# Kernel tuning notes

Hardware: AMD Instinct MI355X
Metric: run time of the kernel (lower is better)

Reference implementation:

```python
import jax, jax.numpy as jnp
import numpy as np

B, N, NH, H = 32, 512, 4, 32      # batch, agents per group, heads, hidden per head
IN_DIM, OUT_DIM = 128, 128
BIG = 9.0e15
SQRT_DK = float(np.sqrt(H))


def setup_inputs() -> dict:
    key = jax.random.key(0)
    keys = iter(jax.random.split(key, 64))

    def nrm(shape, scale=0.05):
        return jax.random.normal(next(keys), shape, dtype=jnp.float32) * scale

    inp = {}
    inp["x0"] = jax.random.normal(next(keys), (B, N, IN_DIM), dtype=jnp.float32)
    inp["x1"] = jax.random.normal(next(keys), (B, N, IN_DIM), dtype=jnp.float32)
    for name in ("m00", "m01", "m10", "m11"):
        inp[name] = jax.random.randint(next(keys), (B, N, N), 0, 2, dtype=jnp.int32)
    # per-group q/k/v projections: Linear(in_dim, NH*H)
    for g in (0, 1):
        inp[f"wq{g}"] = nrm((IN_DIM, NH * H)); inp[f"bq{g}"] = nrm((NH * H,))
        inp[f"wk{g}"] = nrm((IN_DIM, NH * H)); inp[f"bk{g}"] = nrm((NH * H,))
        inp[f"wv{g}"] = nrm((IN_DIM, NH * H)); inp[f"bv{g}"] = nrm((NH * H,))
    # fc_outs[i][j]: Linear(NH*H, H)
    for i in (0, 1):
        for j in (0, 1):
            inp[f"wo{i}{j}"] = nrm((NH * H, H)); inp[f"bo{i}{j}"] = nrm((H,))
    # fc_out_final[i]: Linear(H * 2, out_dim)
    for g in (0, 1):
        inp[f"wf{g}"] = nrm((2 * H, OUT_DIM)); inp[f"bf{g}"] = nrm((OUT_DIM,))
    return inp


def _qkv(x, wq, bq, wk, bk, wv, bv):
    q = jax.nn.relu(x @ wq + bq)
    k = jax.nn.relu(x @ wk + bk)
    v = jax.nn.relu(x @ wv + bv)
    return q, k, v


def _split_heads(t):
    # [B, N, NH*H] -> [B, NH, N, H]; contiguous H-blocks == torch per-head slices
    return t.reshape(B, t.shape[1], NH, H).transpose(0, 2, 1, 3)


def _attend(q, k, v, mask, gate):
    qh, kh, vh = _split_heads(q), _split_heads(k), _split_heads(v)
    logits = jnp.einsum('bhqd,bhkd->bhqk', qh, kh) / SQRT_DK
    m = mask.astype(logits.dtype)[:, None]            # [B,1,Nq,Nk]
    w = jax.nn.softmax(logits * m - BIG * (1.0 - m), axis=-1)
    if gate:
        has = (mask.sum(axis=-1) > 0).astype(w.dtype)  # [B,Nq]
        w = w * has[:, None, :, None]
    out = jnp.einsum('bhqk,bhkd->bhqd', w, vh)
    # heads concatenated along feature dim (matches torch.cat of head slices)
    return out.transpose(0, 2, 1, 3).reshape(B, q.shape[1], NH * H)


def reference(x0, x1, m00, m01, m10, m11,
              wq0, bq0, wk0, bk0, wv0, bv0,
              wq1, bq1, wk1, bk1, wv1, bv1,
              wo00, bo00, wo01, bo01, wo10, bo10, wo11, bo11,
              wf0, bf0, wf1, bf1):
    q0, k0, v0 = _qkv(x0, wq0, bq0, wk0, bk0, wv0, bv0)
    q1, k1, v1 = _qkv(x1, wq1, bq1, wk1, bk1, wv1, bv1)
    inner0 = jax.nn.relu(_attend(q0, k0, v0, m00, gate=False) @ wo00 + bo00)
    inner1 = jax.nn.relu(_attend(q1, k1, v1, m11, gate=False) @ wo11 + bo11)
    inter0 = jax.nn.relu(_attend(q0, k1, v1, m01, gate=True) @ wo01 + bo01)
    inter1 = jax.nn.relu(_attend(q1, k0, v0, m10, gate=True) @ wo10 + bo10)
    out0 = jnp.concatenate([inner0, inter0], axis=-1) @ wf0 + bf0
    out1 = jnp.concatenate([inner1, inter1], axis=-1) @ wf1 + bf1
    return (out0, out1)
```

## Files before the change

kernel.cpp:

```cpp
#include <hip/hip_runtime.h>

#define B_    32
#define N_    512
#define D_    128
#define ROWS  (B_ * N_)
#define SCALE_ 0.17677669529663687f

typedef __bf16 bf16x8 __attribute__((ext_vector_type(8)));
typedef __bf16 bf16x4 __attribute__((ext_vector_type(4)));
typedef float  f32x4  __attribute__((ext_vector_type(4)));

static __device__ __forceinline__ f32x4 mfma16(bf16x8 a, bf16x8 b, f32x4 c) {
  return __builtin_amdgcn_mfma_f32_16x16x32_bf16(a, b, c, 0, 0, 0);
}

__global__ __launch_bounds__(256) void prep_kernel(
    const int* __restrict__ m00, const int* __restrict__ m01,
    const int* __restrict__ m10, const int* __restrict__ m11,
    const float* __restrict__ wq0, const float* __restrict__ wk0, const float* __restrict__ wv0,
    const float* __restrict__ wq1, const float* __restrict__ wk1, const float* __restrict__ wv1,
    const float* __restrict__ wo00, const float* __restrict__ wo01,
    const float* __restrict__ wo10, const float* __restrict__ wo11,
    const float* __restrict__ wf0, const float* __restrict__ wf1,
    __bf16* __restrict__ wtb, __bf16* __restrict__ wob, __bf16* __restrict__ wfb,
    unsigned long long* __restrict__ mpk)
{
  const int bx = blockIdx.x, t = threadIdx.x;
  if (bx < 2048) {
    const int wid = bx * 4 + (t >> 6);
    const int lane = t & 63;
    const int rg = wid & 7, ch = (wid >> 3) & 7, b = (wid >> 6) & 31, a = wid >> 11;
    const int* msel = (a == 0) ? m00 : (a == 1) ? m11 : (a == 2) ? m01 : m10;
    const int* src = msel + ((size_t)b * N_ + rg * 64) * N_ + ch * 64 + lane;
    unsigned long long mine = 0;
    #pragma unroll 8
    for (int it = 0; it < 64; ++it) {
      int v = src[(size_t)it * N_];
      unsigned long long bits = __ballot(v != 0);
      if (it == lane) mine = bits;
    }
    mpk[((size_t)(a * 32 + b) * 8 + ch) * 512 + rg * 64 + lane] = mine;
  } else if (bx < 2054) {
    const int mat = bx - 2048;
    const float* w = (mat == 0) ? wq0 : (mat == 1) ? wk0 : (mat == 2) ? wv0
                   : (mat == 3) ? wq1 : (mat == 4) ? wk1 : wv1;
    __bf16* dst = wtb + mat * 16384;
    for (int idx = t; idx < 16384; idx += 256) {
      const int k = idx >> 7, n = idx & 127;
      dst[n * 128 + k] = (__bf16)w[idx];
    }
  } else if (bx < 2058) {
    const int i = bx - 2054;
    const float* w = (i == 0) ? wo00 : (i == 1) ? wo11 : (i == 2) ? wo01 : wo10;
    __bf16* dst = wob + i * 4096;
    for (int idx = t; idx < 4096; idx += 256) {
      const int k = idx >> 5, n = idx & 31;
      dst[n * 128 + k] = (__bf16)w[idx];
    }
  } else {
    const int g = bx - 2058;
    const float* w = g ? wf1 : wf0;
    __bf16* dst = wfb + g * 8192;
    for (int idx = t; idx < 8192; idx += 256) {
      const int n = idx >> 6, k = idx & 63;
      dst[n * 64 + k] = (__bf16)w[(size_t)k * 128 + n];
    }
  }
}

__global__ __launch_bounds__(256) void qkv_kernel(
    const float* __restrict__ x0, const float* __restrict__ x1,
    const float* __restrict__ bq0, const float* __restrict__ bk0, const float* __restrict__ bv0,
    const float* __restrict__ bq1, const float* __restrict__ bk1, const float* __restrict__ bv1,
    const __bf16* __restrict__ wtb, __bf16* __restrict__ qkvb)
{
  __shared__ __align__(16) __bf16 vtile[128][72];
  const int bx = blockIdx.x;
  const int g = bx >> 8, tile = bx & 255, R0 = tile * 64;
  const int t = threadIdx.x, lane = t & 63, wave = t >> 6;
  const int quad = lane >> 4, ln = lane & 15;
  const float* xs = g ? x1 : x0;

  bf16x8 af[4];
  {
    const int row = R0 + wave * 16 + ln;
    #pragma unroll
    for (int ks = 0; ks < 4; ++ks) {
      const float4* xp = (const float4*)(xs + (size_t)row * D_ + ks * 32 + quad * 8);
      float4 a = xp[0], b = xp[1];
      bf16x8 v;
      v[0] = (__bf16)a.x; v[1] = (__bf16)a.y; v[2] = (__bf16)a.z; v[3] = (__bf16)a.w;
      v[4] = (__bf16)b.x; v[5] = (__bf16)b.y; v[6] = (__bf16)b.z; v[7] = (__bf16)b.w;
      af[ks] = v;
    }
  }
  const f32x4 zero4 = {0.f, 0.f, 0.f, 0.f};

  for (int m = 0; m < 3; ++m) {
    const __bf16* wt = wtb + (g * 3 + m) * 16384;
    const float* bias = (g == 0) ? ((m == 0) ? bq0 : (m == 1) ? bk0 : bv0)
                                 : ((m == 0) ? bq1 : (m == 1) ? bk1 : bv1);
    __bf16* outp = qkvb + (size_t)(g * 3 + m) * (ROWS * D_);

    f32x4 acc[8];
    #pragma unroll
    for (int nt = 0; nt < 8; ++nt) acc[nt] = zero4;
    #pragma unroll
    for (int ks = 0; ks < 4; ++ks) {
      #pragma unroll
      for (int nt = 0; nt < 8; ++nt) {
        bf16x8 bfrag = *(const bf16x8*)(wt + (size_t)(nt * 16 + ln) * D_ + ks * 32 + quad * 8);
        acc[nt] = mfma16(af[ks], bfrag, acc[nt]);
      }
    }

    if (m != 2) {
      const float sc = (m == 0) ? SCALE_ : 1.0f;
      #pragma unroll
      for (int nt = 0; nt < 8; ++nt) {
        const int col = nt * 16 + ln;
        const float bv = bias[col];
        #pragma unroll
        for (int r = 0; r < 4; ++r) {
          float v = fmaxf(acc[nt][r] + bv, 0.f) * sc;
          outp[(size_t)(R0 + wave * 16 + quad * 4 + r) * D_ + col] = (__bf16)v;
        }
      }
    } else {
      #pragma unroll
      for (int nt = 0; nt < 8; ++nt) {
        const int col = nt * 16 + ln;
        const float bv = bias[col];
        #pragma unroll
        for (int r = 0; r < 4; ++r) {
          float v = fmaxf(acc[nt][r] + bv, 0.f);
          vtile[col][wave * 16 + quad * 4 + r] = (__bf16)v;
        }
      }
      __syncthreads();
      const int b = R0 >> 9, kb2 = R0 & 511;
      const int dim = t >> 1, off = (t & 1) * 32;
      uint4* dst = (uint4*)(outp + (size_t)b * (D_ * N_) + (size_t)dim * N_ + kb2 + off);
      const uint4* srcp = (const uint4*)&vtile[dim][off];
      #pragma unroll
      for (int i = 0; i < 4; ++i) dst[i] = srcp[i];
      __syncthreads();
    }
  }
}

__global__ __launch_bounds__(256, 2) void attn_kernel(
    const __bf16* __restrict__ qkvb,
    const unsigned long long* __restrict__ mpk,
    const __bf16* __restrict__ wob,
    const float* __restrict__ bo00, const float* __restrict__ bo01,
    const float* __restrict__ bo10, const float* __restrict__ bo11,
    __bf16* __restrict__ projb)
{
  __shared__ __align__(16) __bf16 raw[18432];

  const int bx = blockIdx.x;
  const int qt = bx >> 7, cb = bx & 127, a = cb >> 5, b = cb & 31;
  const int t = threadIdx.x, lane = t & 63, h = t >> 6;
  const int quad = lane >> 4, ln = lane & 15;

  const int qg = (a == 1 || a == 3) ? 1 : 0;
  const int kg = (a == 1 || a == 2) ? 1 : 0;
  const float* bo = (a == 0) ? bo00 : (a == 1) ? bo11 : (a == 2) ? bo01 : bo10;

  const __bf16* qb  = qkvb + (size_t)(qg * 3 + 0) * (ROWS * D_) + (size_t)(b * N_ + qt * 64) * D_;
  const __bf16* kb  = qkvb + (size_t)(kg * 3 + 1) * (ROWS * D_) + (size_t)b * N_ * D_;
  const __bf16* vtb = qkvb + (size_t)(kg * 3 + 2) * (ROWS * D_) + (size_t)b * D_ * N_;
  const unsigned long long* mrow = mpk + (size_t)(a * 32 + b) * 8 * 512 + qt * 64;

  __bf16* PT = raw + h * 4608;

  bf16x8 qf[4];
  #pragma unroll
  for (int bt = 0; bt < 4; ++bt)
    qf[bt] = *(const bf16x8*)(qb + (size_t)(bt * 16 + ln) * D_ + h * 32 + quad * 8);

  const f32x4 zero4 = {0.f, 0.f, 0.f, 0.f};
  f32x4 Oacc[2][4];
  float lp[4];
  #pragma unroll
  for (int bt = 0; bt < 4; ++bt) {
    lp[bt] = 0.f;
    Oacc[0][bt] = zero4; Oacc[1][bt] = zero4;
  }

  for (int ch = 0; ch < 8; ++ch) {
    const int kc = ch * 64;

    unsigned long long mb[4];
    #pragma unroll
    for (int bt = 0; bt < 4; ++bt)
      mb[bt] = mrow[(size_t)ch * 512 + bt * 16 + ln];

    #pragma unroll
    for (int at = 0; at < 4; ++at) {
      bf16x8 kf = *(const bf16x8*)(kb + (size_t)(kc + at * 16 + ln) * D_ + h * 32 + quad * 8);
      #pragma unroll
      for (int bt = 0; bt < 4; ++bt) {
        f32x4 s = mfma16(kf, qf[bt], zero4);
        bf16x4 pv;
        float ps = 0.f;
        #pragma unroll
        for (int r = 0; r < 4; ++r) {
          const int bit = (int)((mb[bt] >> (at * 16 + quad * 4 + r)) & 1ull);
          const float p = bit ? __expf(s[r]) : 0.f;
          ps += p;
          pv[r] = (__bf16)p;
        }
        lp[bt] += ps;
        *(bf16x4*)&PT[(bt * 16 + ln) * 72 + at * 16 + quad * 4] = pv;
      }
    }

    #pragma unroll
    for (int s2 = 0; s2 < 2; ++s2) {
      bf16x8 pb[4];
      #pragma unroll
      for (int bt = 0; bt < 4; ++bt)
        pb[bt] = *(const bf16x8*)&PT[(bt * 16 + ln) * 72 + s2 * 32 + quad * 8];
      #pragma unroll
      for (int d = 0; d < 2; ++d) {
        bf16x8 vf = *(const bf16x8*)(vtb + (size_t)(h * 32 + d * 16 + ln) * N_ + kc + s2 * 32 + quad * 8);
        #pragma unroll
        for (int bt = 0; bt < 4; ++bt)
          Oacc[d][bt] = mfma16(vf, pb[bt], Oacc[d][bt]);
      }
    }
  }

  float fac[4];
  #pragma unroll
  for (int bt = 0; bt < 4; ++bt) {
    float l = lp[bt] + __shfl_xor(lp[bt], 16);
    l += __shfl_xor(l, 32);
    fac[bt] = (l > 0.f) ? 1.f / l : 0.f;
  }

  __syncthreads();
  __bf16* OL = raw;
  #pragma unroll
  for (int d = 0; d < 2; ++d)
    #pragma unroll
    for (int bt = 0; bt < 4; ++bt) {
      bf16x4 ov;
      #pragma unroll
      for (int r = 0; r < 4; ++r) ov[r] = (__bf16)(Oacc[d][bt][r] * fac[bt]);
      *(bf16x4*)&OL[(bt * 16 + ln) * 136 + h * 32 + d * 16 + quad * 4] = ov;
    }
  __syncthreads();

  const __bf16* wo = wob + a * 4096;
  f32x4 pacc[2];
  pacc[0] = zero4; pacc[1] = zero4;
  #pragma unroll
  for (int ks = 0; ks < 4; ++ks) {
    bf16x8 afr = *(const bf16x8*)&OL[(h * 16 + ln) * 136 + ks * 32 + quad * 8];
    #pragma unroll
    for (int ct = 0; ct < 2; ++ct) {
      bf16x8 bw = *(const bf16x8*)(wo + (size_t)(ct * 16 + ln) * D_ + ks * 32 + quad * 8);
      pacc[ct] = mfma16(afr, bw, pacc[ct]);
    }
  }
  const int R0g = b * N_ + qt * 64;
  #pragma unroll
  for (int ct = 0; ct < 2; ++ct) {
    const int col = ct * 16 + ln;
    const float bv = bo[col];
    #pragma unroll
    for (int r = 0; r < 4; ++r) {
      const float v = fmaxf(pacc[ct][r] + bv, 0.f);
      projb[(size_t)(a * ROWS + R0g + h * 16 + quad * 4 + r) * 32 + col] = (__bf16)v;
    }
  }
}

__global__ __launch_bounds__(256) void outproj_kernel(
    const __bf16* __restrict__ projb, const __bf16* __restrict__ wfb,
    const float* __restrict__ bf0, const float* __restrict__ bf1,
    float* __restrict__ out)
{
  const int t = threadIdx.x, lane = t & 63, w = t >> 6;
  const int quad = lane >> 4, ln = lane & 15;
  const int row = blockIdx.x * 64 + w * 16;
  const f32x4 zero4 = {0.f, 0.f, 0.f, 0.f};

  #pragma unroll
  for (int g = 0; g < 2; ++g) {
    const float* bfp = g ? bf1 : bf0;
    f32x4 acc[8];
    #pragma unroll
    for (int ct = 0; ct < 8; ++ct) acc[ct] = zero4;
    #pragma unroll
    for (int s = 0; s < 2; ++s) {
      const int asrc = s ? (2 + g) : g;
      bf16x8 afr = *(const bf16x8*)(projb + (size_t)(asrc * ROWS + row + ln) * 32 + quad * 8);
      const __bf16* wb = wfb + g * 8192 + s * 32;
      #pragma unroll
      for (int ct = 0; ct < 8; ++ct) {
        bf16x8 bw = *(const bf16x8*)(wb + (size_t)(ct * 16 + ln) * 64 + quad * 8);
        acc[ct] = mfma16(afr, bw, acc[ct]);
      }
    }
    float* og = out + (size_t)g * (ROWS * D_);
    #pragma unroll
    for (int ct = 0; ct < 8; ++ct) {
      const int col = ct * 16 + ln;
      const float bv = bfp[col];
      #pragma unroll
      for (int r = 0; r < 4; ++r)
        og[(size_t)(row + quad * 4 + r) * D_ + col] = acc[ct][r] + bv;
    }
  }
}

extern "C" void kernel_launch(void* const* d_in, const int* in_sizes, int n_in,
                              void* d_out, int out_size, void* d_ws, size_t ws_size,
                              hipStream_t stream)
{
  const float* x0 = (const float*)d_in[0];
  const float* x1 = (const float*)d_in[1];
  const int* m00 = (const int*)d_in[2];
  const int* m01 = (const int*)d_in[3];
  const int* m10 = (const int*)d_in[4];
  const int* m11 = (const int*)d_in[5];
  const float* wq0 = (const float*)d_in[6];  const float* bq0 = (const float*)d_in[7];
  const float* wk0 = (const float*)d_in[8];  const float* bk0 = (const float*)d_in[9];
  const float* wv0 = (const float*)d_in[10]; const float* bv0 = (const float*)d_in[11];
  const float* wq1 = (const float*)d_in[12]; const float* bq1 = (const float*)d_in[13];
  const float* wk1 = (const float*)d_in[14]; const float* bk1 = (const float*)d_in[15];
  const float* wv1 = (const float*)d_in[16]; const float* bv1 = (const float*)d_in[17];
  const float* wo00 = (const float*)d_in[18]; const float* bo00 = (const float*)d_in[19];
  const float* wo01 = (const float*)d_in[20]; const float* bo01 = (const float*)d_in[21];
  const float* wo10 = (const float*)d_in[22]; const float* bo10 = (const float*)d_in[23];
  const float* wo11 = (const float*)d_in[24]; const float* bo11 = (const float*)d_in[25];
  const float* wf0 = (const float*)d_in[26]; const float* bf0 = (const float*)d_in[27];
  const float* wf1 = (const float*)d_in[28]; const float* bf1 = (const float*)d_in[29];

  __bf16* qkvb = (__bf16*)d_ws;
  __bf16* projb = (__bf16*)((char*)d_ws + 25165824);
  __bf16* wtb  = (__bf16*)((char*)d_ws + 29360128);
  __bf16* wob  = (__bf16*)((char*)d_ws + 29556736);
  __bf16* wfb  = (__bf16*)((char*)d_ws + 29589504);
  unsigned long long* mpk = (unsigned long long*)((char*)d_ws + 29622272);

  prep_kernel<<<dim3(2060), dim3(256), 0, stream>>>(
      m00, m01, m10, m11, wq0, wk0, wv0, wq1, wk1, wv1,
      wo00, wo01, wo10, wo11, wf0, wf1, wtb, wob, wfb, mpk);
  qkv_kernel<<<dim3(512), dim3(256), 0, stream>>>(
      x0, x1, bq0, bk0, bv0, bq1, bk1, bv1, wtb, qkvb);
  attn_kernel<<<dim3(1024), dim3(256), 0, stream>>>(
      qkvb, mpk, wob, bo00, bo01, bo10, bo11, projb);
  outproj_kernel<<<dim3(256), dim3(256), 0, stream>>>(
      projb, wfb, bf0, bf1, (float*)d_out);
}
```

Before: 328.8 us.

## Read int masks directly in attention, drop mask bit-packing pass, use exp2

```diff
diff --git a/kernel.cpp b/kernel.cpp
--- a/kernel.cpp
+++ b/kernel.cpp
@@ -4,7 +4,7 @@
 #define N_    512
 #define D_    128
 #define ROWS  (B_ * N_)
-#define SCALE_ 0.17677669529663687f
+#define SCALE2_ (0.17677669529663687f * 1.4426950408889634f)
 
 typedef __bf16 bf16x8 __attribute__((ext_vector_type(8)));
 typedef __bf16 bf16x4 __attribute__((ext_vector_type(4)));
@@ -15,33 +15,16 @@
 }
 
 __global__ __launch_bounds__(256) void prep_kernel(
-    const int* __restrict__ m00, const int* __restrict__ m01,
-    const int* __restrict__ m10, const int* __restrict__ m11,
     const float* __restrict__ wq0, const float* __restrict__ wk0, const float* __restrict__ wv0,
     const float* __restrict__ wq1, const float* __restrict__ wk1, const float* __restrict__ wv1,
     const float* __restrict__ wo00, const float* __restrict__ wo01,
     const float* __restrict__ wo10, const float* __restrict__ wo11,
     const float* __restrict__ wf0, const float* __restrict__ wf1,
-    __bf16* __restrict__ wtb, __bf16* __restrict__ wob, __bf16* __restrict__ wfb,
-    unsigned long long* __restrict__ mpk)
+    __bf16* __restrict__ wtb, __bf16* __restrict__ wob, __bf16* __restrict__ wfb)
 {
   const int bx = blockIdx.x, t = threadIdx.x;
-  if (bx < 2048) {
-    const int wid = bx * 4 + (t >> 6);
-    const int lane = t & 63;
-    const int rg = wid & 7, ch = (wid >> 3) & 7, b = (wid >> 6) & 31, a = wid >> 11;
-    const int* msel = (a == 0) ? m00 : (a == 1) ? m11 : (a == 2) ? m01 : m10;
-    const int* src = msel + ((size_t)b * N_ + rg * 64) * N_ + ch * 64 + lane;
-    unsigned long long mine = 0;
-    #pragma unroll 8
-    for (int it = 0; it < 64; ++it) {
-      int v = src[(size_t)it * N_];
-      unsigned long long bits = __ballot(v != 0);
-      if (it == lane) mine = bits;
-    }
-    mpk[((size_t)(a * 32 + b) * 8 + ch) * 512 + rg * 64 + lane] = mine;
-  } else if (bx < 2054) {
-    const int mat = bx - 2048;
+  if (bx < 6) {
+    const int mat = bx;
     const float* w = (mat == 0) ? wq0 : (mat == 1) ? wk0 : (mat == 2) ? wv0
                    : (mat == 3) ? wq1 : (mat == 4) ? wk1 : wv1;
     __bf16* dst = wtb + mat * 16384;
@@ -49,8 +32,8 @@
       const int k = idx >> 7, n = idx & 127;
       dst[n * 128 + k] = (__bf16)w[idx];
     }
-  } else if (bx < 2058) {
-    const int i = bx - 2054;
+  } else if (bx < 10) {
+    const int i = bx - 6;
     const float* w = (i == 0) ? wo00 : (i == 1) ? wo11 : (i == 2) ? wo01 : wo10;
     __bf16* dst = wob + i * 4096;
     for (int idx = t; idx < 4096; idx += 256) {
@@ -58,7 +41,7 @@
       dst[n * 128 + k] = (__bf16)w[idx];
     }
   } else {
-    const int g = bx - 2058;
+    const int g = bx - 10;
     const float* w = g ? wf1 : wf0;
     __bf16* dst = wfb + g * 8192;
     for (int idx = t; idx < 8192; idx += 256) {
@@ -115,7 +98,7 @@
     }
 
     if (m != 2) {
-      const float sc = (m == 0) ? SCALE_ : 1.0f;
+      const float sc = (m == 0) ? SCALE2_ : 1.0f;
       #pragma unroll
       for (int nt = 0; nt < 8; ++nt) {
         const int col = nt * 16 + ln;
@@ -144,14 +127,14 @@
       const uint4* srcp = (const uint4*)&vtile[dim][off];
       #pragma unroll
       for (int i = 0; i < 4; ++i) dst[i] = srcp[i];
-      __syncthreads();
     }
   }
 }
 
 __global__ __launch_bounds__(256, 2) void attn_kernel(
     const __bf16* __restrict__ qkvb,
-    const unsigned long long* __restrict__ mpk,
+    const int* __restrict__ m00, const int* __restrict__ m01,
+    const int* __restrict__ m10, const int* __restrict__ m11,
     const __bf16* __restrict__ wob,
     const float* __restrict__ bo00, const float* __restrict__ bo01,
     const float* __restrict__ bo10, const float* __restrict__ bo11,
@@ -166,12 +149,13 @@
 
   const int qg = (a == 1 || a == 3) ? 1 : 0;
   const int kg = (a == 1 || a == 2) ? 1 : 0;
+  const int* msel = (a == 0) ? m00 : (a == 1) ? m11 : (a == 2) ? m01 : m10;
   const float* bo = (a == 0) ? bo00 : (a == 1) ? bo11 : (a == 2) ? bo01 : bo10;
 
   const __bf16* qb  = qkvb + (size_t)(qg * 3 + 0) * (ROWS * D_) + (size_t)(b * N_ + qt * 64) * D_;
   const __bf16* kb  = qkvb + (size_t)(kg * 3 + 1) * (ROWS * D_) + (size_t)b * N_ * D_;
   const __bf16* vtb = qkvb + (size_t)(kg * 3 + 2) * (ROWS * D_) + (size_t)b * D_ * N_;
-  const unsigned long long* mrow = mpk + (size_t)(a * 32 + b) * 8 * 512 + qt * 64;
+  const int* mk = msel + ((size_t)b * N_ + qt * 64) * N_;
 
   __bf16* PT = raw + h * 4608;
 
@@ -192,25 +176,22 @@
   for (int ch = 0; ch < 8; ++ch) {
     const int kc = ch * 64;
 
-    unsigned long long mb[4];
-    #pragma unroll
-    for (int bt = 0; bt < 4; ++bt)
-      mb[bt] = mrow[(size_t)ch * 512 + bt * 16 + ln];
-
     #pragma unroll
     for (int at = 0; at < 4; ++at) {
       bf16x8 kf = *(const bf16x8*)(kb + (size_t)(kc + at * 16 + ln) * D_ + h * 32 + quad * 8);
       #pragma unroll
       for (int bt = 0; bt < 4; ++bt) {
+        const int4 mi = *(const int4*)(mk + (size_t)(bt * 16 + ln) * N_ + kc + at * 16 + quad * 4);
         f32x4 s = mfma16(kf, qf[bt], zero4);
         bf16x4 pv;
         float ps = 0.f;
-        #pragma unroll
-        for (int r = 0; r < 4; ++r) {
-          const int bit = (int)((mb[bt] >> (at * 16 + quad * 4 + r)) & 1ull);
-          const float p = bit ? __expf(s[r]) : 0.f;
-          ps += p;
-          pv[r] = (__bf16)p;
+        {
+          const float p0 = mi.x ? __builtin_amdgcn_exp2f(s[0]) : 0.f;
+          const float p1 = mi.y ? __builtin_amdgcn_exp2f(s[1]) : 0.f;
+          const float p2 = mi.z ? __builtin_amdgcn_exp2f(s[2]) : 0.f;
+          const float p3 = mi.w ? __builtin_amdgcn_exp2f(s[3]) : 0.f;
+          ps = (p0 + p1) + (p2 + p3);
+          pv[0] = (__bf16)p0; pv[1] = (__bf16)p1; pv[2] = (__bf16)p2; pv[3] = (__bf16)p3;
         }
         lp[bt] += ps;
         *(bf16x4*)&PT[(bt * 16 + ln) * 72 + at * 16 + quad * 4] = pv;
@@ -346,15 +327,14 @@
   __bf16* wtb  = (__bf16*)((char*)d_ws + 29360128);
   __bf16* wob  = (__bf16*)((char*)d_ws + 29556736);
   __bf16* wfb  = (__bf16*)((char*)d_ws + 29589504);
-  unsigned long long* mpk = (unsigned long long*)((char*)d_ws + 29622272);
-
-  prep_kernel<<<dim3(2060), dim3(256), 0, stream>>>(
-      m00, m01, m10, m11, wq0, wk0, wv0, wq1, wk1, wv1,
-      wo00, wo01, wo10, wo11, wf0, wf1, wtb, wob, wfb, mpk);
+
+  prep_kernel<<<dim3(12), dim3(256), 0, stream>>>(
+      wq0, wk0, wv0, wq1, wk1, wv1, wo00, wo01, wo10, wo11, wf0, wf1,
+      wtb, wob, wfb);
   qkv_kernel<<<dim3(512), dim3(256), 0, stream>>>(
       x0, x1, bq0, bk0, bv0, bq1, bk1, bv1, wtb, qkvb);
   attn_kernel<<<dim3(1024), dim3(256), 0, stream>>>(
-      qkvb, mpk, wob, bo00, bo01, bo10, bo11, projb);
+      qkvb, m00, m01, m10, m11, wob, bo00, bo01, bo10, bo11, projb);
   outproj_kernel<<<dim3(256), dim3(256), 0, stream>>>(
       projb, wfb, bf0, bf1, (float*)d_out);
 }
```

New measurement: 379.0 us. 15.3% more time.
